# Kernel tuning notes

Hardware: AMD Instinct MI355X
Metric: run time of the kernel (lower is better)

## Reference

```python
import jax, jax.numpy as jnp
import numpy as np

H = 16  # heads
EPS_LN = 1e-5

def _ln(x, g, b):
    m = jnp.mean(x, axis=-1, keepdims=True)
    v = jnp.mean((x - m) ** 2, axis=-1, keepdims=True)
    return (x - m) / jnp.sqrt(v + EPS_LN) * g + b

def setup_inputs() -> dict:
    key = jax.random.key(0)
    B, L, d, mlp = 4, 4096, 1024, 4096
    ks = jax.random.split(key, 12)
    s = 0.02
    inp = {
        'x':   jax.random.normal(ks[0], (B, L, d), jnp.float32),
        'Wq':  jax.random.normal(ks[1], (d, d), jnp.float32) * s,
        'bq':  jnp.zeros((d,), jnp.float32),
        'gq':  jnp.ones((d,), jnp.float32),
        'betaq': jnp.zeros((d,), jnp.float32),
        'Wk':  jax.random.normal(ks[2], (d, d), jnp.float32) * s,
        'bk':  jnp.zeros((d,), jnp.float32),
        'gk':  jnp.ones((d,), jnp.float32),
        'betak': jnp.zeros((d,), jnp.float32),
        'Wv':  jax.random.normal(ks[3], (d, d), jnp.float32) * s,
        'bv':  jnp.zeros((d,), jnp.float32),
        'gv':  jnp.ones((d,), jnp.float32),
        'betav': jnp.zeros((d,), jnp.float32),
        'Wfq': jax.random.normal(ks[4], (d, d), jnp.float32) * s,
        'bfq': jnp.zeros((d,), jnp.float32),
        'Wfk': jax.random.normal(ks[5], (d, d), jnp.float32) * s,
        'bfk': jnp.zeros((d,), jnp.float32),
        'ga':  jnp.ones((d,), jnp.float32),
        'ba':  jnp.zeros((d,), jnp.float32),
        'W1':  jax.random.normal(ks[6], (d, mlp), jnp.float32) * s,
        'b1':  jnp.zeros((mlp,), jnp.float32),
        'W2':  jax.random.normal(ks[7], (mlp, d), jnp.float32) * s,
        'b2':  jnp.zeros((d,), jnp.float32),
    }
    return inp

def _fwd(x, Wq, bq, gq, betaq, Wk, bk, gk, betak, Wv, bv, gv, betav,
         Wfq, bfq, Wfk, bfk, ga, ba, W1, b1, W2, b2):
    B, L, d = x.shape
    D = d // H
    # Q/K/V projections + LayerNorm (dropout is eval-mode identity)
    Q = _ln(x @ Wq + bq, gq, betaq)                      # [B,L,d]
    Kc = _ln(x @ Wk + bk, gk, betak)                     # [B,L,d]
    Vc = _ln(x @ Wv + bv, gv, betav)                     # [B,L,d]
    # prepend zero token to K and V (add_zero_token=True)
    z = jnp.zeros((B, 1, d), x.dtype)
    K = jnp.concatenate([z, Kc], axis=1)                 # [B,Lk,d], Lk=L+1
    V = jnp.concatenate([z, Vc], axis=1)
    # kernel feature maps: tanh(Linear(.)) + 1
    phi_Q = jnp.tanh(Q @ Wfq + bfq) + 1.0
    phi_K = jnp.tanh(K @ Wfk + bfk) + 1.0
    split = lambda t: t.reshape(B, t.shape[1], H, D).transpose(0, 2, 1, 3)
    Qh, Kh, Vh = split(Q), split(K), split(V)            # [B,H,L(,k),D]
    pQ, pK = split(phi_Q), split(phi_K)
    # probe-softmax gating of phi_K
    q_probe = jnp.mean(Qh, axis=2) / jnp.sqrt(jnp.asarray(D, x.dtype))  # [B,H,D]
    score = jax.nn.softmax(jnp.einsum('bhd,bhkd->bhk', q_probe, Kh), axis=-1)  # [B,H,Lk]
    pKw = pK * score[..., None]                          # [B,H,Lk,D]
    # linear-attention fast path
    KV = jnp.einsum('bhkd,bhke->bhde', pKw, Vh)          # [B,H,D,D]
    Ksum = jnp.sum(pKw, axis=2)                          # [B,H,D]
    num = jnp.einsum('bhqd,bhde->bhqe', pQ, KV)          # [B,H,L,D]
    den = jnp.einsum('bhqd,bhd->bhq', pQ, Ksum)[..., None] + 1e-6
    out = num / den                                      # [B,H,L,D]
    out = out.transpose(0, 2, 1, 3).reshape(B, L, d)     # merge heads
    a = _ln(out, ga, ba)                                 # attn_norm
    # Residual MLP: a + Linear2(GELU(Linear1(a)))  (exact erf GELU)
    h = a + (jax.nn.gelu(a @ W1 + b1, approximate=False) @ W2 + b2)
    return h + x                                         # outer residual

def reference(x, Wq, bq, gq, betaq, Wk, bk, gk, betak, Wv, bv, gv, betav,
              Wfq, bfq, Wfk, bfk, ga, ba, W1, b1, W2, b2):
    return _fwd(x, Wq, bq, gq, betaq, Wk, bk, gk, betak, Wv, bv, gv, betav,
                Wfq, bfq, Wfk, bfk, ga, ba, W1, b1, W2, b2)
```

## Files before the change

### kernel.cpp

```cpp
#include <hip/hip_runtime.h>
#include <cstddef>
#include <cstdint>

static constexpr int Bc   = 4;
static constexpr int Lq   = 4096;
static constexpr int Dm   = 1024;
static constexpr int Dmlp = 4096;
static constexpr int Mrows = Bc * Lq;
static constexpr int Lk1   = Lq + 1;

typedef unsigned short u16;
typedef __bf16 bf16_t;
typedef bf16_t bf16x8 __attribute__((ext_vector_type(8)));
typedef float  f32x4  __attribute__((ext_vector_type(4)));

__device__ __forceinline__ u16 f2b(float f) {
    uint32_t u = __builtin_bit_cast(uint32_t, f);
    return (u16)((u + 0x7FFFu + ((u >> 16) & 1u)) >> 16);
}
__device__ __forceinline__ float b2f(u16 h) {
    uint32_t u = ((uint32_t)h) << 16;
    return __builtin_bit_cast(float, u);
}

#define GLL16(gsrc, ldst) \
    __builtin_amdgcn_global_load_lds( \
        (const __attribute__((address_space(1))) void*)(gsrc), \
        (__attribute__((address_space(3))) void*)(ldst), 16, 0, 0)

__global__ __launch_bounds__(256)
void zero_kernel(float* __restrict__ p, int n) {
    const int i = blockIdx.x * 256 + threadIdx.x;
    if (i < n) p[i] = 0.0f;
}

__global__ __launch_bounds__(256)
void cvt_bf16_kernel(const float* __restrict__ in, u16* __restrict__ outp, int n) {
    for (int i = (blockIdx.x * 256 + threadIdx.x) * 4; i < n; i += gridDim.x * 256 * 4) {
        float4 v = *(const float4*)&in[i];
        ushort4 o = { f2b(v.x), f2b(v.y), f2b(v.z), f2b(v.w) };
        *(ushort4*)&outp[i] = o;
    }
}

__global__ __launch_bounds__(256)
void transpose_bf16_kernel(const float* __restrict__ in, u16* __restrict__ outp,
                           int R, int C) {
    __shared__ float tile[64][65];
    const int r0 = blockIdx.y * 64, c0 = blockIdx.x * 64;
    const int t = threadIdx.x;
    const int lr = t >> 2, lc0 = (t & 3) * 16;
    #pragma unroll
    for (int j = 0; j < 4; ++j) {
        float4 v = *(const float4*)&in[(size_t)(r0 + lr) * C + c0 + lc0 + j * 4];
        tile[lr][lc0 + j * 4 + 0] = v.x;
        tile[lr][lc0 + j * 4 + 1] = v.y;
        tile[lr][lc0 + j * 4 + 2] = v.z;
        tile[lr][lc0 + j * 4 + 3] = v.w;
    }
    __syncthreads();
    const int oc = t >> 2, rr0 = (t & 3) * 16;
    union { u16 u[16]; uint4 v[2]; } pk;
    #pragma unroll
    for (int j = 0; j < 16; ++j) pk.u[j] = f2b(tile[rr0 + j][oc]);
    u16* po = &outp[(size_t)(c0 + oc) * R + r0 + rr0];
    *(uint4*)&po[0] = pk.v[0];
    *(uint4*)&po[8] = pk.v[1];
}

__global__ __launch_bounds__(256)
void kvt_cvt_kernel(const float* __restrict__ KV, u16* __restrict__ KVT) {
    const int bh = blockIdx.x;
    __shared__ float t[64][65];
    const int tid = threadIdx.x;
    const int r = tid >> 2, c0 = (tid & 3) * 16;
    const float* src = &KV[(size_t)bh * 4096];
    #pragma unroll
    for (int j = 0; j < 4; ++j) {
        float4 v = *(const float4*)&src[r * 64 + c0 + j * 4];
        t[r][c0 + j * 4 + 0] = v.x;
        t[r][c0 + j * 4 + 1] = v.y;
        t[r][c0 + j * 4 + 2] = v.z;
        t[r][c0 + j * 4 + 3] = v.w;
    }
    __syncthreads();
    const int e = tid >> 2, d0 = (tid & 3) * 16;
    union { u16 u[16]; uint4 v[2]; } pk;
    #pragma unroll
    for (int j = 0; j < 16; ++j) pk.u[j] = f2b(t[d0 + j][e]);
    u16* po = &KVT[(size_t)bh * 4096 + e * 64 + d0];
    *(uint4*)&po[0] = pk.v[0];
    *(uint4*)&po[8] = pk.v[1];
}

template<int ACT, bool RES, bool ACCUM, bool BIAS, bool OBF16>
__global__ __launch_bounds__(256, 2)
void mfma_gemm256(const u16* __restrict__ A, int ldA,
                  const u16* __restrict__ Bt, int ldB,
                  const float* __restrict__ bias,
                  void* __restrict__ Cout,
                  const u16* __restrict__ res1, const float* __restrict__ res2,
                  int M, int N, int K) {
    __shared__ u16 As[8192];
    __shared__ u16 Bs[4096];
    const int tid = threadIdx.x;
    const int l   = tid & 63;
    const int w   = tid >> 6;
    const int wm  = w >> 1;
    const int wn  = w & 1;
    const int l16 = l & 15, l4 = l >> 4;

    const int gx = N >> 7;
    int bid = blockIdx.x;
    bid = (bid & 7) * ((int)gridDim.x >> 3) + (bid >> 3);
    const int brow = (bid / gx) << 8;
    const int bcol = (bid % gx) << 7;

    const int srow = tid >> 2;
    const int skof = ((tid & 3) ^ ((tid >> 3) & 3)) << 3;
    const u16* gA = A  + (size_t)(brow + srow) * ldA + skof;
    const u16* gB = Bt + (size_t)(bcol + srow) * ldB + skof;
    const size_t gsA = (size_t)64 * ldA;
    const size_t gsB = (size_t)64 * ldB;
    u16* lA = As + tid * 8;
    u16* lB = Bs + tid * 8;

    const int koff_rd = ((l4 ^ ((l16 >> 1) & 3)) << 3);
    const int aRdBase = (wm * 128 + l16) * 32 + koff_rd;
    const int bRdBase = (wn * 64  + l16) * 32 + koff_rd;

    f32x4 acc[8][4];
    const f32x4 zf = {0.f, 0.f, 0.f, 0.f};
    #pragma unroll
    for (int m = 0; m < 8; ++m)
        #pragma unroll
        for (int n = 0; n < 4; ++n) acc[m][n] = zf;

    const int T = K >> 5;
    for (int t = 0; t < T; ++t) {
        GLL16(gA,           lA);
        GLL16(gA +     gsA, lA + 2048);
        GLL16(gA + 2 * gsA, lA + 4096);
        GLL16(gA + 3 * gsA, lA + 6144);
        GLL16(gB,           lB);
        GLL16(gB +     gsB, lB + 2048);
        gA += 32; gB += 32;
        __syncthreads();
        bf16x8 bfr[4], afr[8];
        #pragma unroll
        for (int n = 0; n < 4; ++n)
            bfr[n] = *(const bf16x8*)&Bs[bRdBase + n * 512];
        #pragma unroll
        for (int m = 0; m < 8; ++m)
            afr[m] = *(const bf16x8*)&As[aRdBase + m * 512];
        #pragma unroll
        for (int m = 0; m < 8; ++m)
            #pragma unroll
            for (int n = 0; n < 4; ++n)
                acc[m][n] = __builtin_amdgcn_mfma_f32_16x16x32_bf16(
                    afr[m], bfr[n], acc[m][n], 0, 0, 0);
        __syncthreads();
    }

    float bvn[4];
    int coln[4];
    #pragma unroll
    for (int n = 0; n < 4; ++n) {
        coln[n] = bcol + wn * 64 + n * 16 + l16;
        bvn[n] = BIAS ? bias[coln[n]] : 0.f;
    }
    #pragma unroll
    for (int m = 0; m < 8; ++m) {
        #pragma unroll
        for (int q = 0; q < 4; ++q) {
            const size_t row = (size_t)brow + wm * 128 + m * 16 + l4 * 4 + q;
            #pragma unroll
            for (int n = 0; n < 4; ++n) {
                float v = acc[m][n][q] + bvn[n];
                if (ACT == 1) v = tanhf(v) + 1.0f;
                if (ACT == 2) v = 0.5f * v * (1.0f + erff(v * 0.70710678118654752f));
                const size_t idx = row * (size_t)N + coln[n];
                if (OBF16) {
                    ((u16*)Cout)[idx] = f2b(v);
                } else {
                    float* Cf = (float*)Cout;
                    if (ACCUM) v += Cf[idx];
                    if (RES)   v += b2f(res1[idx]) + res2[idx];
                    Cf[idx] = v;
                }
            }
        }
    }
}

__global__ __launch_bounds__(256)
void ln1024_bf16_kernel(const u16* __restrict__ in, u16* __restrict__ outp,
                        const float* __restrict__ g, const float* __restrict__ be) {
    const size_t base = (size_t)blockIdx.x * Dm;
    const int tid = threadIdx.x;
    ushort4 raw = *(const ushort4*)&in[base + tid * 4];
    float v0 = b2f(raw.x), v1 = b2f(raw.y), v2 = b2f(raw.z), v3 = b2f(raw.w);
    float s  = v0 + v1 + v2 + v3;
    float sq = v0 * v0 + v1 * v1 + v2 * v2 + v3 * v3;
    #pragma unroll
    for (int off = 32; off > 0; off >>= 1) {
        s  += __shfl_down(s,  off, 64);
        sq += __shfl_down(sq, off, 64);
    }
    __shared__ float rs[4], rq[4];
    const int lane = tid & 63, wv = tid >> 6;
    if (lane == 0) { rs[wv] = s; rq[wv] = sq; }
    __syncthreads();
    s  = rs[0] + rs[1] + rs[2] + rs[3];
    sq = rq[0] + rq[1] + rq[2] + rq[3];
    const float mean = s * (1.0f / 1024.0f);
    const float var  = sq * (1.0f / 1024.0f) - mean * mean;
    const float inv  = rsqrtf(var + 1e-5f);
    float4 gv = *(const float4*)&g[tid * 4];
    float4 bv = *(const float4*)&be[tid * 4];
    ushort4 o;
    o.x = f2b((v0 - mean) * inv * gv.x + bv.x);
    o.y = f2b((v1 - mean) * inv * gv.y + bv.y);
    o.z = f2b((v2 - mean) * inv * gv.z + bv.z);
    o.w = f2b((v3 - mean) * inv * gv.w + bv.w);
    *(ushort4*)&outp[base + tid * 4] = o;
}

__global__ __launch_bounds__(256)
void qprobe_kernel(const u16* __restrict__ Q, float* __restrict__ qp) {
    const int b = blockIdx.z;
    const int col = blockIdx.x * 256 + threadIdx.x;
    const int lchunk = Lq / 16;
    const int l0 = blockIdx.y * lchunk;
    const u16* p = Q + ((size_t)b * Lq + l0) * Dm + col;
    float s = 0.f;
    for (int l = 0; l < lchunk; ++l, p += Dm) s += b2f(*p);
    atomicAdd(&qp[b * Dm + col], s * (1.0f / (4096.0f * 8.0f)));
}

__global__ __launch_bounds__(256)
void logits_kernel(const u16* __restrict__ Kc, const float* __restrict__ qp,
                   float* __restrict__ score) {
    const int bh = blockIdx.y, b = bh >> 4, h = bh & 15;
    __shared__ float q[64];
    if (threadIdx.x < 64) q[threadIdx.x] = qp[b * Dm + h * 64 + threadIdx.x];
    __syncthreads();
    const int kr = blockIdx.x * 256 + threadIdx.x;
    const ushort4* krp = (const ushort4*)&Kc[((size_t)b * Lq + kr) * Dm + h * 64];
    float s = 0.f;
    #pragma unroll
    for (int i = 0; i < 16; ++i) {
        ushort4 v = krp[i];
        s += q[i * 4 + 0] * b2f(v.x) + q[i * 4 + 1] * b2f(v.y)
           + q[i * 4 + 2] * b2f(v.z) + q[i * 4 + 3] * b2f(v.w);
    }
    score[(size_t)bh * Lk1 + kr + 1] = s;
    if (blockIdx.x == 0 && threadIdx.x == 0) score[(size_t)bh * Lk1] = 0.f;
}

__global__ __launch_bounds__(256)
void softmax4097_kernel(float* __restrict__ sc) {
    __shared__ float buf[Lk1];
    __shared__ float red[8];
    const size_t base = (size_t)blockIdx.x * Lk1;
    const int tid = threadIdx.x;
    float mx = -1e30f;
    for (int i = tid; i < Lk1; i += 256) { float v = sc[base + i]; buf[i] = v; mx = fmaxf(mx, v); }
    #pragma unroll
    for (int off = 32; off > 0; off >>= 1) mx = fmaxf(mx, __shfl_down(mx, off, 64));
    const int lane = tid & 63, wv = tid >> 6;
    if (lane == 0) red[wv] = mx;
    __syncthreads();
    mx = fmaxf(fmaxf(red[0], red[1]), fmaxf(red[2], red[3]));
    float sum = 0.f;
    for (int i = tid; i < Lk1; i += 256) { float e = expf(buf[i] - mx); buf[i] = e; sum += e; }
    #pragma unroll
    for (int off = 32; off > 0; off >>= 1) sum += __shfl_down(sum, off, 64);
    if (lane == 0) red[4 + wv] = sum;
    __syncthreads();
    sum = red[4] + red[5] + red[6] + red[7];
    const float inv = 1.0f / sum;
    for (int i = tid; i < Lk1; i += 256) sc[base + i] = buf[i] * inv;
}

__global__ __launch_bounds__(256)
void kv_kernel(const u16* __restrict__ phiK, const u16* __restrict__ Vc,
               const float* __restrict__ sc, float* __restrict__ KV) {
    const int bh = blockIdx.y, b = bh >> 4, h = bh & 15;
    const int lchunk = Lq / 8;
    const int l0 = blockIdx.x * lchunk;
    __shared__ float pk[8][64];
    __shared__ float vv[8][64];
    const int i0 = (threadIdx.x >> 4) << 2;
    const int j0 = (threadIdx.x & 15) << 2;
    float acc[4][4] = {};
    for (int lb = l0; lb < l0 + lchunk; lb += 8) {
        #pragma unroll
        for (int q = 0; q < 2; ++q) {
            const int idx = threadIdx.x + q * 256;
            const int r = idx >> 6, c = idx & 63;
            const float scv = sc[(size_t)bh * Lk1 + lb + r + 1];
            const size_t off = ((size_t)b * Lq + lb + r) * Dm + h * 64 + c;
            pk[r][c] = b2f(phiK[off]) * scv;
            vv[r][c] = b2f(Vc[off]);
        }
        __syncthreads();
        #pragma unroll
        for (int r = 0; r < 8; ++r) {
            float ra[4], rb[4];
            #pragma unroll
            for (int i = 0; i < 4; ++i) ra[i] = pk[r][i0 + i];
            #pragma unroll
            for (int j = 0; j < 4; ++j) rb[j] = vv[r][j0 + j];
            #pragma unroll
            for (int i = 0; i < 4; ++i)
                #pragma unroll
                for (int j = 0; j < 4; ++j)
                    acc[i][j] = fmaf(ra[i], rb[j], acc[i][j]);
        }
        __syncthreads();
    }
    #pragma unroll
    for (int i = 0; i < 4; ++i)
        #pragma unroll
        for (int j = 0; j < 4; ++j)
            atomicAdd(&KV[((size_t)bh * 64 + i0 + i) * 64 + j0 + j], acc[i][j]);
}

__global__ __launch_bounds__(64)
void ksum_kernel(const u16* __restrict__ phiK, const float* __restrict__ sc,
                 const float* __restrict__ bfk, float* __restrict__ Ksum) {
    const int bh = blockIdx.y, b = bh >> 4, h = bh & 15;
    const int lchunk = Lq / 8;
    const int l0 = blockIdx.x * lchunk;
    const int dd = threadIdx.x;
    float s = 0.f;
    const u16* pp = &phiK[((size_t)b * Lq + l0) * Dm + h * 64 + dd];
    const float* sp = &sc[(size_t)bh * Lk1 + l0 + 1];
    for (int l = 0; l < lchunk; ++l, pp += Dm) s = fmaf(b2f(*pp), sp[l], s);
    if (blockIdx.x == 0) s += sc[(size_t)bh * Lk1] * (tanhf(bfk[h * 64 + dd]) + 1.0f);
    atomicAdd(&Ksum[bh * 64 + dd], s);
}

__global__ __launch_bounds__(256, 2)
void attnout_mfma_kernel(const u16* __restrict__ phiQ, const u16* __restrict__ KVT,
                         const float* __restrict__ Ksum, u16* __restrict__ outp) {
    __shared__ u16 pqs[256 * 64];
    __shared__ float kss[64];
    __shared__ float dns[256];
    const int bh = blockIdx.y, b = bh >> 4, h = bh & 15;
    const int l0 = blockIdx.x * 256;
    const int tid = threadIdx.x;
    const int l = tid & 63, w = tid >> 6;
    const int l16 = l & 15, l4 = l >> 4;

    bf16x8 bfr[4][2];
    {
        const u16* kb = KVT + (size_t)bh * 4096;
        #pragma unroll
        for (int n = 0; n < 4; ++n)
            #pragma unroll
            for (int kk = 0; kk < 2; ++kk)
                bfr[n][kk] = *(const bf16x8*)&kb[(n * 16 + l16) * 64 + kk * 32 + l4 * 8];
    }
    if (tid < 64) kss[tid] = Ksum[bh * 64 + tid];

    {
        const int rsub = tid >> 3;
        const int ssrc = ((tid & 7) ^ (rsub & 7)) * 8;
        u16* ldst = &pqs[(size_t)tid * 8];
        #pragma unroll
        for (int j = 0; j < 8; ++j) {
            const u16* g = phiQ + (((size_t)(b * Lq + l0 + j * 32 + rsub)) << 10)
                          + h * 64 + ssrc;
            GLL16(g, ldst + j * 2048);
        }
    }
    __syncthreads();

    {
        const int r7 = tid & 7;
        float s = 0.f;
        #pragma unroll
        for (int sl = 0; sl < 8; ++sl) {
            bf16x8 v = *(const bf16x8*)&pqs[tid * 64 + ((sl ^ r7) << 3)];
            #pragma unroll
            for (int j = 0; j < 8; ++j) s = fmaf(b2f(((u16*)&v)[j]), kss[sl * 8 + j], s);
        }
        dns[tid] = 1.0f / (s + 1e-6f);
    }

    f32x4 acc[4][4];
    const f32x4 zf = {0.f, 0.f, 0.f, 0.f};
    #pragma unroll
    for (int m = 0; m < 4; ++m)
        #pragma unroll
        for (int n = 0; n < 4; ++n) acc[m][n] = zf;
    #pragma unroll
    for (int kk = 0; kk < 2; ++kk) {
        bf16x8 afr[4];
        #pragma unroll
        for (int m = 0; m < 4; ++m) {
            const int row = w * 64 + m * 16 + l16;
            afr[m] = *(const bf16x8*)&pqs[row * 64 + (((kk * 4 + l4) ^ (row & 7)) << 3)];
        }
        #pragma unroll
        for (int m = 0; m < 4; ++m)
            #pragma unroll
            for (int n = 0; n < 4; ++n)
                acc[m][n] = __builtin_amdgcn_mfma_f32_16x16x32_bf16(
                    afr[m], bfr[n][kk], acc[m][n], 0, 0, 0);
    }
    __syncthreads();

    #pragma unroll
    for (int m = 0; m < 4; ++m) {
        #pragma unroll
        for (int q = 0; q < 4; ++q) {
            const int rl = w * 64 + m * 16 + l4 * 4 + q;
            const float dn = dns[rl];
            const size_t rowg = ((size_t)(b * Lq + l0 + rl)) << 10;
            #pragma unroll
            for (int n = 0; n < 4; ++n)
                outp[rowg + h * 64 + n * 16 + l16] = f2b(acc[m][n][q] * dn);
        }
    }
}

extern "C" void kernel_launch(void* const* d_in, const int* in_sizes, int n_in,
                              void* d_out, int out_size, void* d_ws, size_t ws_size,
                              hipStream_t stream) {
    const float* x     = (const float*)d_in[0];
    const float* Wq    = (const float*)d_in[1];
    const float* bq    = (const float*)d_in[2];
    const float* gq    = (const float*)d_in[3];
    const float* betaq = (const float*)d_in[4];
    const float* Wk    = (const float*)d_in[5];
    const float* bk    = (const float*)d_in[6];
    const float* gk    = (const float*)d_in[7];
    const float* betak = (const float*)d_in[8];
    const float* Wv    = (const float*)d_in[9];
    const float* bv    = (const float*)d_in[10];
    const float* gv    = (const float*)d_in[11];
    const float* betav = (const float*)d_in[12];
    const float* Wfq   = (const float*)d_in[13];
    const float* bfq   = (const float*)d_in[14];
    const float* Wfk   = (const float*)d_in[15];
    const float* bfk   = (const float*)d_in[16];
    const float* ga    = (const float*)d_in[17];
    const float* ba    = (const float*)d_in[18];
    const float* W1    = (const float*)d_in[19];
    const float* b1    = (const float*)d_in[20];
    const float* W2    = (const float*)d_in[21];
    const float* b2    = (const float*)d_in[22];
    float* outp = (float*)d_out;

    uint8_t* wsb = (uint8_t*)d_ws;
    size_t off = 0;
    auto alloc = [&](size_t bytes) { void* p = wsb + off; off += bytes; return p; };
    const size_t Md = (size_t)Mrows * Dm;
    u16* B0   = (u16*)alloc(Md * 2);
    u16* B1   = (u16*)alloc(Md * 2);
    u16* B2   = (u16*)alloc(Md * 2);
    u16* Wtq  = (u16*)alloc((size_t)Dm * Dm * 2);
    u16* Wtk  = (u16*)alloc((size_t)Dm * Dm * 2);
    u16* Wtv  = (u16*)alloc((size_t)Dm * Dm * 2);
    u16* Wtfq = (u16*)alloc((size_t)Dm * Dm * 2);
    u16* Wtfk = (u16*)alloc((size_t)Dm * Dm * 2);
    u16* Wt1  = (u16*)alloc((size_t)Dm * Dmlp * 2);
    u16* Wt2  = (u16*)alloc((size_t)Dm * Dmlp * 2);
    float* qp    = (float*)alloc(4096 * 4);
    float* KV    = (float*)alloc((size_t)64 * 64 * 64 * 4);
    float* Ksum  = (float*)alloc(4096 * 4);
    float* score = (float*)alloc((size_t)64 * Lk1 * 4);
    u16* KVT     = (u16*)alloc((size_t)64 * 64 * 64 * 2);
    u16* PK = (u16*)outp;
    u16* PQ = (u16*)outp + Md;

    const dim3 blk(256);
    const dim3 gP(512);
    const dim3 gM1(1024);

    cvt_bf16_kernel<<<2048, blk, 0, stream>>>(x, B0, (int)Md);
    transpose_bf16_kernel<<<dim3(16, 16), blk, 0, stream>>>(Wq,  Wtq,  Dm, Dm);
    transpose_bf16_kernel<<<dim3(16, 16), blk, 0, stream>>>(Wk,  Wtk,  Dm, Dm);
    transpose_bf16_kernel<<<dim3(16, 16), blk, 0, stream>>>(Wv,  Wtv,  Dm, Dm);
    transpose_bf16_kernel<<<dim3(16, 16), blk, 0, stream>>>(Wfq, Wtfq, Dm, Dm);
    transpose_bf16_kernel<<<dim3(16, 16), blk, 0, stream>>>(Wfk, Wtfk, Dm, Dm);
    transpose_bf16_kernel<<<dim3(64, 16), blk, 0, stream>>>(W1,  Wt1,  Dm, Dmlp);
    transpose_bf16_kernel<<<dim3(16, 64), blk, 0, stream>>>(W2,  Wt2,  Dmlp, Dm);
    {
        const int nz = 4096 + 64 * 64 * 64 + 4096;
        zero_kernel<<<(nz + 255) / 256, blk, 0, stream>>>(qp, nz);
    }

    mfma_gemm256<0, false, false, true, true><<<gP, blk, 0, stream>>>(
        B0, Dm, Wtq, Dm, bq, B1, nullptr, nullptr, Mrows, Dm, Dm);
    ln1024_bf16_kernel<<<Mrows, blk, 0, stream>>>(B1, B1, gq, betaq);
    mfma_gemm256<0, false, false, true, true><<<gP, blk, 0, stream>>>(
        B0, Dm, Wtk, Dm, bk, B2, nullptr, nullptr, Mrows, Dm, Dm);
    ln1024_bf16_kernel<<<Mrows, blk, 0, stream>>>(B2, B2, gk, betak);

    qprobe_kernel<<<dim3(Dm / 256, 16, Bc), blk, 0, stream>>>(B1, qp);
    logits_kernel<<<dim3(Lq / 256, 64), blk, 0, stream>>>(B2, qp, score);
    softmax4097_kernel<<<64, blk, 0, stream>>>(score);

    mfma_gemm256<1, false, false, true, true><<<gP, blk, 0, stream>>>(
        B2, Dm, Wtfk, Dm, bfk, PK, nullptr, nullptr, Mrows, Dm, Dm);
    mfma_gemm256<1, false, false, true, true><<<gP, blk, 0, stream>>>(
        B1, Dm, Wtfq, Dm, bfq, PQ, nullptr, nullptr, Mrows, Dm, Dm);

    mfma_gemm256<0, false, false, true, true><<<gP, blk, 0, stream>>>(
        B0, Dm, Wtv, Dm, bv, B1, nullptr, nullptr, Mrows, Dm, Dm);
    ln1024_bf16_kernel<<<Mrows, blk, 0, stream>>>(B1, B1, gv, betav);

    kv_kernel<<<dim3(8, 64), blk, 0, stream>>>(PK, B1, score, KV);
    ksum_kernel<<<dim3(8, 64), dim3(64), 0, stream>>>(PK, score, bfk, Ksum);
    kvt_cvt_kernel<<<64, blk, 0, stream>>>(KV, KVT);

    attnout_mfma_kernel<<<dim3(Lq / 256, 64), blk, 0, stream>>>(PQ, KVT, Ksum, B2);
    ln1024_bf16_kernel<<<Mrows, blk, 0, stream>>>(B2, B2, ga, ba);

    u16* H1 = B0;
    for (int c = 0; c < 2; ++c) {
        mfma_gemm256<2, false, false, true, true><<<gM1, blk, 0, stream>>>(
            B2, Dm, Wt1 + (size_t)c * 2048 * Dm, Dm, b1 + c * 2048,
            H1, nullptr, nullptr, Mrows, 2048, Dm);
        if (c == 0) {
            mfma_gemm256<0, false, false, true, false><<<gP, blk, 0, stream>>>(
                H1, 2048, Wt2 + (size_t)c * 2048, Dmlp, b2,
                outp, nullptr, nullptr, Mrows, Dm, 2048);
        } else {
            mfma_gemm256<0, true, true, false, false><<<gP, blk, 0, stream>>>(
                H1, 2048, Wt2 + (size_t)c * 2048, Dmlp, nullptr,
                outp, B2, x, Mrows, Dm, 2048);
        }
    }
}
```

Measured before the change: 850.5 us.

## Prelayout weights in MFMA fragment order and load B straight to registers

```diff
diff --git a/kernel.cpp b/kernel.cpp
--- a/kernel.cpp
+++ b/kernel.cpp
@@ -44,28 +44,38 @@
 }
 
 __global__ __launch_bounds__(256)
-void transpose_bf16_kernel(const float* __restrict__ in, u16* __restrict__ outp,
-                           int R, int C) {
+void wfrag_cvt_kernel(const float* __restrict__ W, u16* __restrict__ Wf,
+                      int K, int N) {
     __shared__ float tile[64][65];
-    const int r0 = blockIdx.y * 64, c0 = blockIdx.x * 64;
+    const int c0 = blockIdx.x * 64, k0 = blockIdx.y * 64;
     const int t = threadIdx.x;
-    const int lr = t >> 2, lc0 = (t & 3) * 16;
+    const int kr = t >> 2, cc0 = (t & 3) * 16;
     #pragma unroll
     for (int j = 0; j < 4; ++j) {
-        float4 v = *(const float4*)&in[(size_t)(r0 + lr) * C + c0 + lc0 + j * 4];
-        tile[lr][lc0 + j * 4 + 0] = v.x;
-        tile[lr][lc0 + j * 4 + 1] = v.y;
-        tile[lr][lc0 + j * 4 + 2] = v.z;
-        tile[lr][lc0 + j * 4 + 3] = v.w;
-    }
-    __syncthreads();
-    const int oc = t >> 2, rr0 = (t & 3) * 16;
-    union { u16 u[16]; uint4 v[2]; } pk;
-    #pragma unroll
-    for (int j = 0; j < 16; ++j) pk.u[j] = f2b(tile[rr0 + j][oc]);
-    u16* po = &outp[(size_t)(c0 + oc) * R + r0 + rr0];
-    *(uint4*)&po[0] = pk.v[0];
-    *(uint4*)&po[8] = pk.v[1];
+        float4 v = *(const float4*)&W[(size_t)(k0 + kr) * N + c0 + cc0 + j * 4];
+        tile[kr][cc0 + j * 4 + 0] = v.x;
+        tile[kr][cc0 + j * 4 + 1] = v.y;
+        tile[kr][cc0 + j * 4 + 2] = v.z;
+        tile[kr][cc0 + j * 4 + 3] = v.w;
+    }
+    __syncthreads();
+    const int KB = K >> 5;
+    const int ch = t >> 5;
+    const int fbn = ch >> 1, fbk = ch & 1;
+    const int nb = (c0 >> 4) + fbn;
+    const int kb = (k0 >> 5) + fbk;
+    #pragma unroll
+    for (int q = 0; q < 2; ++q) {
+        const int l = ((t & 31) << 1) | q;
+        union { u16 u[8]; uint4 v; } pk;
+        #pragma unroll
+        for (int j = 0; j < 8; ++j) {
+            const int kl = fbk * 32 + (l >> 4) * 8 + j;
+            const int cl = fbn * 16 + (l & 15);
+            pk.u[j] = f2b(tile[kl][cl]);
+        }
+        *(uint4*)&Wf[(((size_t)nb * KB + kb) * 64 + l) * 8] = pk.v;
+    }
 }
 
 __global__ __launch_bounds__(256)
@@ -94,40 +104,38 @@
 }
 
 template<int ACT, bool RES, bool ACCUM, bool BIAS, bool OBF16>
-__global__ __launch_bounds__(256, 2)
-void mfma_gemm256(const u16* __restrict__ A, int ldA,
-                  const u16* __restrict__ Bt, int ldB,
+__global__ __launch_bounds__(512, 1)
+void mfma_gemm_rb(const u16* __restrict__ A, int ldA,
+                  const u16* __restrict__ Wf, int kbStride,
                   const float* __restrict__ bias,
                   void* __restrict__ Cout,
                   const u16* __restrict__ res1, const float* __restrict__ res2,
                   int M, int N, int K) {
-    __shared__ u16 As[8192];
-    __shared__ u16 Bs[4096];
+    __shared__ u16 As[2][8192];
     const int tid = threadIdx.x;
     const int l   = tid & 63;
     const int w   = tid >> 6;
-    const int wm  = w >> 1;
-    const int wn  = w & 1;
+    const int wm  = w >> 2;
+    const int wn  = w & 3;
     const int l16 = l & 15, l4 = l >> 4;
 
-    const int gx = N >> 7;
+    const int gx = N >> 8;
     int bid = blockIdx.x;
     bid = (bid & 7) * ((int)gridDim.x >> 3) + (bid >> 3);
     const int brow = (bid / gx) << 8;
-    const int bcol = (bid % gx) << 7;
-
-    const int srow = tid >> 2;
-    const int skof = ((tid & 3) ^ ((tid >> 3) & 3)) << 3;
-    const u16* gA = A  + (size_t)(brow + srow) * ldA + skof;
-    const u16* gB = Bt + (size_t)(bcol + srow) * ldB + skof;
-    const size_t gsA = (size_t)64 * ldA;
-    const size_t gsB = (size_t)64 * ldB;
-    u16* lA = As + tid * 8;
-    u16* lB = Bs + tid * 8;
+    const int bcol = (bid % gx) << 8;
+
+    const int srow = w * 16 + (l >> 2);
+    const int skof = ((l & 3) ^ ((l >> 3) & 3)) << 3;
+    const u16* gA = A + (size_t)(brow + srow) * ldA + skof;
+    const size_t gsA = (size_t)128 * ldA;
+    const int ldst = w * 512 + l * 8;
 
     const int koff_rd = ((l4 ^ ((l16 >> 1) & 3)) << 3);
     const int aRdBase = (wm * 128 + l16) * 32 + koff_rd;
-    const int bRdBase = (wn * 64  + l16) * 32 + koff_rd;
+
+    const u16* wb = Wf + ((size_t)((bcol >> 4) + wn * 4) * kbStride) * 512
+                       + (size_t)l * 8;
 
     f32x4 acc[8][4];
     const f32x4 zf = {0.f, 0.f, 0.f, 0.f};
@@ -136,29 +144,40 @@
         #pragma unroll
         for (int n = 0; n < 4; ++n) acc[m][n] = zf;
 
+    auto stageA = [&](int t, int slot) {
+        const u16* s = gA + (size_t)t * 32;
+        GLL16(s,       &As[slot][ldst]);
+        GLL16(s + gsA, &As[slot][ldst + 4096]);
+    };
+
     const int T = K >> 5;
+    stageA(0, 0);
+    bf16x8 bc[4], bnx[4];
+    #pragma unroll
+    for (int n = 0; n < 4; ++n)
+        bc[n] = *(const bf16x8*)(wb + (size_t)n * kbStride * 512);
+    __syncthreads();
+
     for (int t = 0; t < T; ++t) {
-        GLL16(gA,           lA);
-        GLL16(gA +     gsA, lA + 2048);
-        GLL16(gA + 2 * gsA, lA + 4096);
-        GLL16(gA + 3 * gsA, lA + 6144);
-        GLL16(gB,           lB);
-        GLL16(gB +     gsB, lB + 2048);
-        gA += 32; gB += 32;
-        __syncthreads();
-        bf16x8 bfr[4], afr[8];
-        #pragma unroll
-        for (int n = 0; n < 4; ++n)
-            bfr[n] = *(const bf16x8*)&Bs[bRdBase + n * 512];
+        if (t + 1 < T) {
+            #pragma unroll
+            for (int n = 0; n < 4; ++n)
+                bnx[n] = *(const bf16x8*)(wb + ((size_t)n * kbStride + t + 1) * 512);
+            stageA(t + 1, (t + 1) & 1);
+        }
+        const u16* Acur = As[t & 1];
+        bf16x8 afr[8];
         #pragma unroll
         for (int m = 0; m < 8; ++m)
-            afr[m] = *(const bf16x8*)&As[aRdBase + m * 512];
+            afr[m] = *(const bf16x8*)&Acur[aRdBase + m * 512];
         #pragma unroll
         for (int m = 0; m < 8; ++m)
             #pragma unroll
             for (int n = 0; n < 4; ++n)
                 acc[m][n] = __builtin_amdgcn_mfma_f32_16x16x32_bf16(
-                    afr[m], bfr[n], acc[m][n], 0, 0, 0);
+                    afr[m], bc[n], acc[m][n], 0, 0, 0);
+        #pragma unroll
+        for (int n = 0; n < 4; ++n) bc[n] = bnx[n];
         __syncthreads();
     }
 
@@ -462,13 +481,13 @@
     u16* B0   = (u16*)alloc(Md * 2);
     u16* B1   = (u16*)alloc(Md * 2);
     u16* B2   = (u16*)alloc(Md * 2);
-    u16* Wtq  = (u16*)alloc((size_t)Dm * Dm * 2);
-    u16* Wtk  = (u16*)alloc((size_t)Dm * Dm * 2);
-    u16* Wtv  = (u16*)alloc((size_t)Dm * Dm * 2);
-    u16* Wtfq = (u16*)alloc((size_t)Dm * Dm * 2);
-    u16* Wtfk = (u16*)alloc((size_t)Dm * Dm * 2);
-    u16* Wt1  = (u16*)alloc((size_t)Dm * Dmlp * 2);
-    u16* Wt2  = (u16*)alloc((size_t)Dm * Dmlp * 2);
+    u16* Wfq_ = (u16*)alloc((size_t)Dm * Dm * 2);
+    u16* Wfk_ = (u16*)alloc((size_t)Dm * Dm * 2);
+    u16* Wfv_ = (u16*)alloc((size_t)Dm * Dm * 2);
+    u16* Wffq = (u16*)alloc((size_t)Dm * Dm * 2);
+    u16* Wffk = (u16*)alloc((size_t)Dm * Dm * 2);
+    u16* Wf1  = (u16*)alloc((size_t)Dm * Dmlp * 2);
+    u16* Wf2  = (u16*)alloc((size_t)Dm * Dmlp * 2);
     float* qp    = (float*)alloc(4096 * 4);
     float* KV    = (float*)alloc((size_t)64 * 64 * 64 * 4);
     float* Ksum  = (float*)alloc(4096 * 4);
@@ -478,40 +497,44 @@
     u16* PQ = (u16*)outp + Md;
 
     const dim3 blk(256);
-    const dim3 gP(512);
-    const dim3 gM1(1024);
+    const dim3 blk512(512);
+    const dim3 gA(256);
+    const dim3 gM(512);
 
     cvt_bf16_kernel<<<2048, blk, 0, stream>>>(x, B0, (int)Md);
-    transpose_bf16_kernel<<<dim3(16, 16), blk, 0, stream>>>(Wq,  Wtq,  Dm, Dm);
-    transpose_bf16_kernel<<<dim3(16, 16), blk, 0, stream>>>(Wk,  Wtk,  Dm, Dm);
-    transpose_bf16_kernel<<<dim3(16, 16), blk, 0, stream>>>(Wv,  Wtv,  Dm, Dm);
-    transpose_bf16_kernel<<<dim3(16, 16), blk, 0, stream>>>(Wfq, Wtfq, Dm, Dm);
-    transpose_bf16_kernel<<<dim3(16, 16), blk, 0, stream>>>(Wfk, Wtfk, Dm, Dm);
-    transpose_bf16_kernel<<<dim3(64, 16), blk, 0, stream>>>(W1,  Wt1,  Dm, Dmlp);
-    transpose_bf16_kernel<<<dim3(16, 64), blk, 0, stream>>>(W2,  Wt2,  Dmlp, Dm);
+    wfrag_cvt_kernel<<<dim3(16, 16), blk, 0, stream>>>(Wq,  Wfq_, Dm, Dm);
+    wfrag_cvt_kernel<<<dim3(16, 16), blk, 0, stream>>>(Wk,  Wfk_, Dm, Dm);
+    wfrag_cvt_kernel<<<dim3(16, 16), blk, 0, stream>>>(Wv,  Wfv_, Dm, Dm);
+    wfrag_cvt_kernel<<<dim3(16, 16), blk, 0, stream>>>(Wfq, Wffq, Dm, Dm);
+    wfrag_cvt_kernel<<<dim3(16, 16), blk, 0, stream>>>(Wfk, Wffk, Dm, Dm);
+    wfrag_cvt_kernel<<<dim3(64, 16), blk, 0, stream>>>(W1,  Wf1,  Dm, Dmlp);
+    wfrag_cvt_kernel<<<dim3(16, 64), blk, 0, stream>>>(W2,  Wf2,  Dmlp, Dm);
     {
         const int nz = 4096 + 64 * 64 * 64 + 4096;
         zero_kernel<<<(nz + 255) / 256, blk, 0, stream>>>(qp, nz);
     }
 
-    mfma_gemm256<0, false, false, true, true><<<gP, blk, 0, stream>>>(
-        B0, Dm, Wtq, Dm, bq, B1, nullptr, nullptr, Mrows, Dm, Dm);
+    const int KB1 = Dm >> 5;
+    const int KB2 = Dmlp >> 5;
+
+    mfma_gemm_rb<0, false, false, true, true><<<gA, blk512, 0, stream>>>(
+        B0, Dm, Wfq_, KB1, bq, B1, nullptr, nullptr, Mrows, Dm, Dm);
     ln1024_bf16_kernel<<<Mrows, blk, 0, stream>>>(B1, B1, gq, betaq);
-    mfma_gemm256<0, false, false, true, true><<<gP, blk, 0, stream>>>(
-        B0, Dm, Wtk, Dm, bk, B2, nullptr, nullptr, Mrows, Dm, Dm);
+    mfma_gemm_rb<0, false, false, true, true><<<gA, blk512, 0, stream>>>(
+        B0, Dm, Wfk_, KB1, bk, B2, nullptr, nullptr, Mrows, Dm, Dm);
     ln1024_bf16_kernel<<<Mrows, blk, 0, stream>>>(B2, B2, gk, betak);
 
     qprobe_kernel<<<dim3(Dm / 256, 16, Bc), blk, 0, stream>>>(B1, qp);
     logits_kernel<<<dim3(Lq / 256, 64), blk, 0, stream>>>(B2, qp, score);
     softmax4097_kernel<<<64, blk, 0, stream>>>(score);
 
-    mfma_gemm256<1, false, false, true, true><<<gP, blk, 0, stream>>>(
-        B2, Dm, Wtfk, Dm, bfk, PK, nullptr, nullptr, Mrows, Dm, Dm);
-    mfma_gemm256<1, false, false, true, true><<<gP, blk, 0, stream>>>(
-        B1, Dm, Wtfq, Dm, bfq, PQ, nullptr, nullptr, Mrows, Dm, Dm);
-
-    mfma_gemm256<0, false, false, true, true><<<gP, blk, 0, stream>>>(
-        B0, Dm, Wtv, Dm, bv, B1, nullptr, nullptr, Mrows, Dm, Dm);
+    mfma_gemm_rb<1, false, false, true, true><<<gA, blk512, 0, stream>>>(
+        B2, Dm, Wffk, KB1, bfk, PK, nullptr, nullptr, Mrows, Dm, Dm);
+    mfma_gemm_rb<1, false, false, true, true><<<gA, blk512, 0, stream>>>(
+        B1, Dm, Wffq, KB1, bfq, PQ, nullptr, nullptr, Mrows, Dm, Dm);
+
+    mfma_gemm_rb<0, false, false, true, true><<<gA, blk512, 0, stream>>>(
+        B0, Dm, Wfv_, KB1, bv, B1, nullptr, nullptr, Mrows, Dm, Dm);
     ln1024_bf16_kernel<<<Mrows, blk, 0, stream>>>(B1, B1, gv, betav);
 
     kv_kernel<<<dim3(8, 64), blk, 0, stream>>>(PK, B1, score, KV);
@@ -523,16 +546,16 @@
 
     u16* H1 = B0;
     for (int c = 0; c < 2; ++c) {
-        mfma_gemm256<2, false, false, true, true><<<gM1, blk, 0, stream>>>(
-            B2, Dm, Wt1 + (size_t)c * 2048 * Dm, Dm, b1 + c * 2048,
+        mfma_gemm_rb<2, false, false, true, true><<<gM, blk512, 0, stream>>>(
+            B2, Dm, Wf1 + (size_t)c * 128 * KB1 * 512, KB1, b1 + c * 2048,
             H1, nullptr, nullptr, Mrows, 2048, Dm);
         if (c == 0) {
-            mfma_gemm256<0, false, false, true, false><<<gP, blk, 0, stream>>>(
-                H1, 2048, Wt2 + (size_t)c * 2048, Dmlp, b2,
+            mfma_gemm_rb<0, false, false, true, false><<<gA, blk512, 0, stream>>>(
+                H1, 2048, Wf2 + (size_t)c * 64 * 512, KB2, b2,
                 outp, nullptr, nullptr, Mrows, Dm, 2048);
         } else {
-            mfma_gemm256<0, true, true, false, false><<<gP, blk, 0, stream>>>(
-                H1, 2048, Wt2 + (size_t)c * 2048, Dmlp, nullptr,
+            mfma_gemm_rb<0, true, true, false, false><<<gA, blk512, 0, stream>>>(
+                H1, 2048, Wf2 + (size_t)c * 64 * 512, KB2, nullptr,
                 outp, B2, x, Mrows, Dm, 2048);
         }
     }
```

Result: slower. 895.6 us (+5.3%).
